# Optimization experiments

Hardware: AMD Instinct MI355X
Metric: run time of the kernel (lower is better)

Reference implementation:

```python
import jax, jax.numpy as jnp
import numpy as np

MARGIN = 0.2
PAIR_EPS = 1e-6   # torch pairwise_distance eps inside TripletMarginLoss
NORM_EPS = 1e-12  # F.normalize eps


def setup_inputs() -> dict:
    key = jax.random.key(0)
    k1, k2, k3 = jax.random.split(key, 3)
    bs, C, D = 64, 1024, 64
    inputs = jax.random.normal(k1, (bs, C, D), dtype=jnp.float32)
    label = jax.random.randint(k2, (bs, C, 1), 0, 2).astype(jnp.float32)
    prot = jax.random.normal(k3, (C, D), dtype=jnp.float32)
    prot = prot / jnp.linalg.norm(prot, axis=1, keepdims=True)
    return {"inputs": inputs, "label": label, "pos_prot": prot, "only_update": 0}


def reference(inputs, label, pos_prot, only_update):
    bs, C, D = inputs.shape
    # F.normalize(p=2, dim=1) per class slice == normalize over last dim of [bs,C,D]
    nrm = jnp.linalg.norm(inputs, axis=-1, keepdims=True)
    x = inputs / jnp.maximum(nrm, NORM_EPS)                      # [bs,C,D]

    # torch.cdist(x, prot): euclidean distances [bs, C(anchor cls), C(prot)]
    x2 = jnp.sum(x * x, axis=-1)                                 # [bs,C]
    p2 = jnp.sum(pos_prot * pos_prot, axis=-1)                   # [C]
    xp = jnp.einsum('bcd,kd->bck', x, pos_prot)                  # [bs,C,C]
    d2 = x2[:, :, None] + p2[None, None, :] - 2.0 * xp
    prot_dist = jnp.sqrt(jnp.maximum(d2, 0.0))                   # [bs,C,C]

    # hard negative: nearest prototype excluding the anchor's own class
    # (argsort + skip-self loop == masked argmin)
    eye = jnp.eye(C, dtype=bool)[None, :, :]
    neg_cls = jnp.argmin(jnp.where(eye, jnp.inf, prot_dist), axis=-1)  # [bs,C]

    positives = pos_prot[None, :, :]                             # [1,C,D] (broadcast of repeat)
    negatives = pos_prot[neg_cls]                                # [bs,C,D]

    # TripletMarginLoss(margin=0.2, p=2, reduction='none'), eps inside distance
    d_ap = jnp.linalg.norm(x - positives + PAIR_EPS, axis=-1)    # [bs,C]
    d_an = jnp.linalg.norm(x - negatives + PAIR_EPS, axis=-1)    # [bs,C]
    tri = jnp.maximum(d_ap - d_an + MARGIN, 0.0)                 # [bs,C]

    w = label[:, :, 0]                                           # [bs,C]
    loss = jnp.mean(jnp.sum(tri * w, axis=-1) / jnp.sum(w, axis=-1))
    return loss
```

## Files before the change

kernel.cpp:

```cpp
#include <hip/hip_runtime.h>
#include <cfloat>

#define BS 64
#define C  1024
#define D  64
#define CT 128
#define NX8 (BS * C * D / 8)

typedef __attribute__((ext_vector_type(8))) short short8;
typedef __attribute__((ext_vector_type(4))) float f32x4;
typedef unsigned short ushort_t;
typedef unsigned int uint_t;

__device__ __forceinline__ ushort_t f2bf(float f) {
    uint_t u = __float_as_uint(f);
    u += 0x7fffu + ((u >> 16) & 1u);
    return (ushort_t)(u >> 16);
}

__global__ __launch_bounds__(256)
void prep_cvt(const float* __restrict__ inputs, const float* __restrict__ prot,
              ushort_t* __restrict__ xhg, ushort_t* __restrict__ phg)
{
    const int idx = blockIdx.x * 256 + threadIdx.x;
    const bool isX = idx < NX8;
    const int rel = isX ? idx : idx - NX8;
    const float* sb = isX ? inputs : prot;
    ushort_t* db = isX ? xhg : phg;

    const int ft = rel >> 7, w = rel & 127, h = w >> 6, ln = w & 63;
    const int rr = ft * 16 + (ln & 15), dg = h * 4 + (ln >> 4);
    const float* s = sb + (size_t)rr * D + dg * 8;
    float4 a = *(const float4*)s;
    float4 b2 = *(const float4*)(s + 4);
    float x[8] = {a.x, a.y, a.z, a.w, b2.x, b2.y, b2.z, b2.w};
    short8 hv;
    #pragma unroll
    for (int e = 0; e < 8; e++) hv[e] = (short)f2bf(x[e]);
    ((short8*)db)[rel] = hv;
}

__global__ __launch_bounds__(512, 4)
void triplet_mfma(const float* __restrict__ inputs,
                  const float* __restrict__ label,
                  const float* __restrict__ prot,
                  const ushort_t* __restrict__ xhg,
                  const ushort_t* __restrict__ phg,
                  float* __restrict__ part)
{
    __shared__ uint_t redk[CT][4];
    __shared__ float  wred[16];

    const int tid  = threadIdx.x;
    const int lane = tid & 63;
    const int wid  = tid >> 6;
    const int wr   = wid >> 2;
    const int wc   = wid & 3;
    const int b    = blockIdx.x >> 3;
    const int c0   = (blockIdx.x & 7) * CT;

    const short8* BH = (const short8*)phg;
    const short8* XH = (const short8*)xhg;

    short8 ta0 = BH[(size_t)(wc * 16 + 0) * 128 + lane];
    short8 ta1 = BH[(size_t)(wc * 16 + 0) * 128 + 64 + lane];
    short8 tb0 = BH[(size_t)(wc * 16 + 1) * 128 + lane];
    short8 tb1 = BH[(size_t)(wc * 16 + 1) * 128 + 64 + lane];

    const size_t ftb = (size_t)blockIdx.x * 8 + wr * 4;
    short8 ah[4][2];
    #pragma unroll
    for (int i = 0; i < 4; i++) {
        ah[i][0] = XH[(ftb + i) * 128 + lane];
        ah[i][1] = XH[(ftb + i) * 128 + 64 + lane];
    }

    uint_t bestk[16];
    #pragma unroll
    for (int q = 0; q < 16; q++) bestk[q] = 0u;

    const uint_t MMASK = 0xFFFFFC00u;
    const int rowtile0 = (c0 >> 4) + wr * 4;
    const int rsub = (lane >> 4) * 4;
    const int csub = lane & 15;

    auto process = [&](int jt, short8 b0, short8 b1) {
        const int jg = wc * 16 + jt;
        const uint_t cidx = (uint_t)(1023 - (jg * 16 + csub));
        #pragma unroll
        for (int i = 0; i < 4; i++) {
            f32x4 acc = {16.f, 16.f, 16.f, 16.f};
            acc = __builtin_amdgcn_mfma_f32_16x16x32_bf16(ah[i][0], b0, acc, 0, 0, 0);
            acc = __builtin_amdgcn_mfma_f32_16x16x32_bf16(ah[i][1], b1, acc, 0, 0, 0);
            const bool dtile = (rowtile0 + i) == jg;
            #pragma unroll
            for (int r = 0; r < 4; r++) {
                uint_t key = (__float_as_uint(acc[r]) & MMASK) | cidx;
                if (dtile && (rsub + r) == csub) key = 0u;
                bestk[i * 4 + r] = bestk[i * 4 + r] > key ? bestk[i * 4 + r] : key;
            }
        }
    };

    for (int jt = 0; jt < 16; jt += 2) {
        const int p0 = (jt + 2 < 16) ? jt + 2 : 15;
        const int p1 = (jt + 3 < 16) ? jt + 3 : 15;
        short8 n0 = BH[(size_t)(wc * 16 + p0) * 128 + lane];
        short8 n1 = BH[(size_t)(wc * 16 + p0) * 128 + 64 + lane];
        __builtin_amdgcn_sched_barrier(0);
        process(jt, ta0, ta1);
        short8 m0 = BH[(size_t)(wc * 16 + p1) * 128 + lane];
        short8 m1 = BH[(size_t)(wc * 16 + p1) * 128 + 64 + lane];
        __builtin_amdgcn_sched_barrier(0);
        process(jt + 1, tb0, tb1);
        ta0 = n0; ta1 = n1; tb0 = m0; tb1 = m1;
    }

    #pragma unroll
    for (int i = 0; i < 4; i++)
        #pragma unroll
        for (int r = 0; r < 4; r++) {
            uint_t v = bestk[i * 4 + r];
            #pragma unroll
            for (int off = 1; off < 16; off <<= 1) {
                uint_t ov = (uint_t)__shfl_xor((int)v, off);
                v = v > ov ? v : ov;
            }
            if (csub == 0) redk[wr * 64 + i * 16 + rsub + r][wc] = v;
        }
    __syncthreads();

    float num = 0.f, den = 0.f;
    {
        const int row = tid >> 2, p4 = tid & 3;
        uint_t kk = redk[row][p4];
        {
            uint_t o1 = (uint_t)__shfl_xor((int)kk, 1); kk = kk > o1 ? kk : o1;
            uint_t o2 = (uint_t)__shfl_xor((int)kk, 2); kk = kk > o2 ? kk : o2;
        }
        const int bi = 1023 - (int)(kk & 0x3FFu);
        const int cg = c0 + row;

        const float4* xr = (const float4*)(inputs + (size_t)(b * C + cg) * D) + p4 * 4;
        float4 xv[4];
        float x2 = 0.f;
        #pragma unroll
        for (int q = 0; q < 4; q++) {
            xv[q] = xr[q];
            x2 = fmaf(xv[q].x, xv[q].x, fmaf(xv[q].y, xv[q].y,
                 fmaf(xv[q].z, xv[q].z, fmaf(xv[q].w, xv[q].w, x2))));
        }
        x2 += __shfl_xor(x2, 1);
        x2 += __shfl_xor(x2, 2);
        const float inv = 1.0f / fmaxf(sqrtf(x2), 1e-12f);

        const float4* pp = (const float4*)(prot + (size_t)cg * D) + p4 * 4;
        const float4* pn = (const float4*)(prot + (size_t)bi * D) + p4 * 4;
        float sap = 0.f, san = 0.f;
        #pragma unroll
        for (int q = 0; q < 4; q++) {
            float4 aa = pp[q];
            float4 nn = pn[q];
            float t;
            t = fmaf(xv[q].x, inv, -aa.x) + 1e-6f;  sap = fmaf(t, t, sap);
            t = fmaf(xv[q].y, inv, -aa.y) + 1e-6f;  sap = fmaf(t, t, sap);
            t = fmaf(xv[q].z, inv, -aa.z) + 1e-6f;  sap = fmaf(t, t, sap);
            t = fmaf(xv[q].w, inv, -aa.w) + 1e-6f;  sap = fmaf(t, t, sap);
            t = fmaf(xv[q].x, inv, -nn.x) + 1e-6f;  san = fmaf(t, t, san);
            t = fmaf(xv[q].y, inv, -nn.y) + 1e-6f;  san = fmaf(t, t, san);
            t = fmaf(xv[q].z, inv, -nn.z) + 1e-6f;  san = fmaf(t, t, san);
            t = fmaf(xv[q].w, inv, -nn.w) + 1e-6f;  san = fmaf(t, t, san);
        }
        sap += __shfl_xor(sap, 1);  sap += __shfl_xor(sap, 2);
        san += __shfl_xor(san, 1);  san += __shfl_xor(san, 2);
        if (p4 == 0) {
            float tri = fmaxf(sqrtf(sap) - sqrtf(san) + 0.2f, 0.0f);
            float w   = label[b * C + cg];
            num = tri * w;
            den = w;
        }
    }

    #pragma unroll
    for (int off = 1; off < 64; off <<= 1) {
        num += __shfl_xor(num, off);
        den += __shfl_xor(den, off);
    }
    if (lane == 0) { wred[wid * 2] = num; wred[wid * 2 + 1] = den; }
    __syncthreads();

    if (tid == 0) {
        float sn = 0.f, sd = 0.f;
        #pragma unroll
        for (int wv = 0; wv < 8; wv++) { sn += wred[wv * 2]; sd += wred[wv * 2 + 1]; }
        part[blockIdx.x * 2 + 0] = sn;
        part[blockIdx.x * 2 + 1] = sd;
    }
}

__global__ void triplet_finish(const float* __restrict__ part, float* __restrict__ out)
{
    int t = threadIdx.x;
    float num = 0.f, den = 0.f;
    #pragma unroll
    for (int h = 0; h < 8; h++) {
        num += part[(t * 8 + h) * 2 + 0];
        den += part[(t * 8 + h) * 2 + 1];
    }
    float v = num / den;
    #pragma unroll
    for (int off = 32; off > 0; off >>= 1) v += __shfl_down(v, off);
    if (t == 0) out[0] = v * (1.0f / (float)BS);
}

extern "C" void kernel_launch(void* const* d_in, const int* in_sizes, int n_in,
                              void* d_out, int out_size, void* d_ws, size_t ws_size,
                              hipStream_t stream)
{
    const float* inputs = (const float*)d_in[0];
    const float* label  = (const float*)d_in[1];
    const float* prot   = (const float*)d_in[2];
    float* out = (float*)d_out;

    ushort_t* xhg  = (ushort_t*)d_ws;
    ushort_t* phg  = xhg + (size_t)BS * C * D;
    float*    part = (float*)(phg + (size_t)C * D);

    prep_cvt<<<dim3((NX8 + C * D / 8) / 256), dim3(256), 0, stream>>>(
        inputs, prot, xhg, phg);
    triplet_mfma<<<dim3(BS * (C / CT)), dim3(512), 0, stream>>>(
        inputs, label, prot, xhg, phg, part);
    triplet_finish<<<1, 64, 0, stream>>>(part, out);
}
```

Measured before the change: 30.38 us.

## Fuse input bf16 conversion into MFMA kernel; prep only prototypes

The input tensor is no longer converted to bf16 in a separate prep pass. Each wave now loads its fp32 anchor rows directly and converts them to bf16 fragments in registers inside the main kernel. This removes a full write and re-read of a 8 MB bf16 copy of the input, and the prep kernel shrinks to converting only the small prototype matrix. In exchange the main kernel issues strided fp32 loads with in-register conversion before its MFMA loop starts.

```diff
diff --git a/kernel.cpp b/kernel.cpp
--- a/kernel.cpp
+++ b/kernel.cpp
@@ -5,7 +5,6 @@
 #define C  1024
 #define D  64
 #define CT 128
-#define NX8 (BS * C * D / 8)
 
 typedef __attribute__((ext_vector_type(8))) short short8;
 typedef __attribute__((ext_vector_type(4))) float f32x4;
@@ -18,33 +17,29 @@
     return (ushort_t)(u >> 16);
 }
 
-__global__ __launch_bounds__(256)
-void prep_cvt(const float* __restrict__ inputs, const float* __restrict__ prot,
-              ushort_t* __restrict__ xhg, ushort_t* __restrict__ phg)
-{
-    const int idx = blockIdx.x * 256 + threadIdx.x;
-    const bool isX = idx < NX8;
-    const int rel = isX ? idx : idx - NX8;
-    const float* sb = isX ? inputs : prot;
-    ushort_t* db = isX ? xhg : phg;
-
-    const int ft = rel >> 7, w = rel & 127, h = w >> 6, ln = w & 63;
-    const int rr = ft * 16 + (ln & 15), dg = h * 4 + (ln >> 4);
-    const float* s = sb + (size_t)rr * D + dg * 8;
-    float4 a = *(const float4*)s;
-    float4 b2 = *(const float4*)(s + 4);
-    float x[8] = {a.x, a.y, a.z, a.w, b2.x, b2.y, b2.z, b2.w};
-    short8 hv;
-    #pragma unroll
-    for (int e = 0; e < 8; e++) hv[e] = (short)f2bf(x[e]);
-    ((short8*)db)[rel] = hv;
+__global__ void prep_prot(const float* __restrict__ prot, ushort_t* __restrict__ ph)
+{
+    const int k = blockIdx.x * 128 + threadIdx.x;
+    const float4* row = (const float4*)(prot + (size_t)k * D);
+    const int jt = k >> 4;
+    #pragma unroll
+    for (int dg = 0; dg < 8; dg++) {
+        float4 a = row[dg * 2];
+        float4 b = row[dg * 2 + 1];
+        float x[8] = {a.x, a.y, a.z, a.w, b.x, b.y, b.z, b.w};
+        short8 hv;
+        #pragma unroll
+        for (int e = 0; e < 8; e++) hv[e] = (short)f2bf(x[e]);
+        const int h  = dg >> 2;
+        const int ln = (k & 15) + (dg & 3) * 16;
+        ((short8*)ph)[(size_t)jt * 128 + h * 64 + ln] = hv;
+    }
 }
 
 __global__ __launch_bounds__(512, 4)
 void triplet_mfma(const float* __restrict__ inputs,
                   const float* __restrict__ label,
                   const float* __restrict__ prot,
-                  const ushort_t* __restrict__ xhg,
                   const ushort_t* __restrict__ phg,
                   float* __restrict__ part)
 {
@@ -60,20 +55,29 @@
     const int c0   = (blockIdx.x & 7) * CT;
 
     const short8* BH = (const short8*)phg;
-    const short8* XH = (const short8*)xhg;
 
     short8 ta0 = BH[(size_t)(wc * 16 + 0) * 128 + lane];
     short8 ta1 = BH[(size_t)(wc * 16 + 0) * 128 + 64 + lane];
     short8 tb0 = BH[(size_t)(wc * 16 + 1) * 128 + lane];
     short8 tb1 = BH[(size_t)(wc * 16 + 1) * 128 + 64 + lane];
 
-    const size_t ftb = (size_t)blockIdx.x * 8 + wr * 4;
+    const float* xbase = inputs + (size_t)(b * C + c0 + wr * 64) * D;
     short8 ah[4][2];
     #pragma unroll
-    for (int i = 0; i < 4; i++) {
-        ah[i][0] = XH[(ftb + i) * 128 + lane];
-        ah[i][1] = XH[(ftb + i) * 128 + 64 + lane];
-    }
+    for (int i = 0; i < 4; i++)
+        #pragma unroll
+        for (int h = 0; h < 2; h++) {
+            const float* s = xbase + (size_t)(i * 16 + (lane & 15)) * D
+                           + (h * 4 + (lane >> 4)) * 8;
+            float4 a  = *(const float4*)s;
+            float4 b2 = *(const float4*)(s + 4);
+            short8 hv;
+            hv[0] = (short)f2bf(a.x);  hv[1] = (short)f2bf(a.y);
+            hv[2] = (short)f2bf(a.z);  hv[3] = (short)f2bf(a.w);
+            hv[4] = (short)f2bf(b2.x); hv[5] = (short)f2bf(b2.y);
+            hv[6] = (short)f2bf(b2.z); hv[7] = (short)f2bf(b2.w);
+            ah[i][h] = hv;
+        }
 
     uint_t bestk[16];
     #pragma unroll
@@ -222,13 +226,11 @@
     const float* prot   = (const float*)d_in[2];
     float* out = (float*)d_out;
 
-    ushort_t* xhg  = (ushort_t*)d_ws;
-    ushort_t* phg  = xhg + (size_t)BS * C * D;
+    ushort_t* phg  = (ushort_t*)d_ws;
     float*    part = (float*)(phg + (size_t)C * D);
 
-    prep_cvt<<<dim3((NX8 + C * D / 8) / 256), dim3(256), 0, stream>>>(
-        inputs, prot, xhg, phg);
+    prep_prot<<<dim3(C / 128), dim3(128), 0, stream>>>(prot, phg);
     triplet_mfma<<<dim3(BS * (C / CT)), dim3(512), 0, stream>>>(
-        inputs, label, prot, xhg, phg, part);
+        inputs, label, prot, phg, part);
     triplet_finish<<<1, 64, 0, stream>>>(part, out);
 }
```

Result: slower. 33.30 us (+9.6%).

## Stage prototype tiles in shared memory in two chunks per block

Applied to the files above, without the earlier changes.

Loads the bf16 prototype matrix cooperatively into a 64KB LDS buffer in two halves, and each wave reads its B tiles from LDS instead of from global memory per wave. This aims to cut redundant global/L2 traffic, since all 8 waves previously fetched prototype tiles independently. The 64KB of LDS limits how many blocks fit per CU, and the block-wide syncs add serialization with no overlap between loading and compute.

```diff
diff --git a/kernel.cpp b/kernel.cpp
--- a/kernel.cpp
+++ b/kernel.cpp
@@ -48,6 +48,7 @@
                   const ushort_t* __restrict__ phg,
                   float* __restrict__ part)
 {
+    __shared__ short8 bsh[32 * 128];
     __shared__ uint_t redk[CT][4];
     __shared__ float  wred[16];
 
@@ -62,11 +63,6 @@
     const short8* BH = (const short8*)phg;
     const short8* XH = (const short8*)xhg;
 
-    short8 ta0 = BH[(size_t)(wc * 16 + 0) * 128 + lane];
-    short8 ta1 = BH[(size_t)(wc * 16 + 0) * 128 + 64 + lane];
-    short8 tb0 = BH[(size_t)(wc * 16 + 1) * 128 + lane];
-    short8 tb1 = BH[(size_t)(wc * 16 + 1) * 128 + 64 + lane];
-
     const size_t ftb = (size_t)blockIdx.x * 8 + wr * 4;
     short8 ah[4][2];
     #pragma unroll
@@ -84,8 +80,7 @@
     const int rsub = (lane >> 4) * 4;
     const int csub = lane & 15;
 
-    auto process = [&](int jt, short8 b0, short8 b1) {
-        const int jg = wc * 16 + jt;
+    auto process = [&](int jg, short8 b0, short8 b1) {
         const uint_t cidx = (uint_t)(1023 - (jg * 16 + csub));
         #pragma unroll
         for (int i = 0; i < 4; i++) {
@@ -102,18 +97,26 @@
         }
     };
 
-    for (int jt = 0; jt < 16; jt += 2) {
-        const int p0 = (jt + 2 < 16) ? jt + 2 : 15;
-        const int p1 = (jt + 3 < 16) ? jt + 3 : 15;
-        short8 n0 = BH[(size_t)(wc * 16 + p0) * 128 + lane];
-        short8 n1 = BH[(size_t)(wc * 16 + p0) * 128 + 64 + lane];
-        __builtin_amdgcn_sched_barrier(0);
-        process(jt, ta0, ta1);
-        short8 m0 = BH[(size_t)(wc * 16 + p1) * 128 + lane];
-        short8 m1 = BH[(size_t)(wc * 16 + p1) * 128 + 64 + lane];
-        __builtin_amdgcn_sched_barrier(0);
-        process(jt + 1, tb0, tb1);
-        ta0 = n0; ta1 = n1; tb0 = m0; tb1 = m1;
+    for (int ch = 0; ch < 2; ch++) {
+        if (ch) __syncthreads();
+        const short8* src = BH + (size_t)ch * 4096;
+        #pragma unroll
+        for (int it = 0; it < 8; it++)
+            bsh[it * 512 + tid] = src[it * 512 + tid];
+        __syncthreads();
+
+        const int base = wc * 8;
+        short8 cb0 = bsh[(base + 0) * 128 + lane];
+        short8 cb1 = bsh[(base + 0) * 128 + 64 + lane];
+        #pragma unroll
+        for (int lt = 0; lt < 8; lt++) {
+            const int nt = (lt + 1 < 8) ? lt + 1 : 7;
+            short8 n0 = bsh[(base + nt) * 128 + lane];
+            short8 n1 = bsh[(base + nt) * 128 + 64 + lane];
+            __builtin_amdgcn_sched_barrier(0);
+            process(ch * 32 + base + lt, cb0, cb1);
+            cb0 = n0; cb1 = n1;
+        }
     }
 
     #pragma unroll
```

New measurement: 28.04 us. 1.08x faster.
